# Kernel tuning notes

Measured on AMD Instinct MI355X. Metric: run time of the kernel, lower is better.

The kernel has to match this reference:

```python
import jax, jax.numpy as jnp
import numpy as np

H = 16  # hidden_size
IN = 1  # input_size

def setup_inputs() -> dict:
    key = jax.random.key(0)
    ks = jax.random.split(key, 7)
    B, T = 2048, 2048
    s_ih = 1.0 / np.sqrt(H)
    return {
        "x": jax.random.normal(ks[0], (B, T, IN), dtype=jnp.float32),
        # PyTorch LSTM param layout: [4H, in] / [4H, H], gate order i,f,g,o
        "W_ih": jax.random.uniform(ks[1], (4 * H, IN), jnp.float32, -s_ih, s_ih),
        "W_hh": jax.random.uniform(ks[2], (4 * H, H), jnp.float32, -s_ih, s_ih),
        "b_ih": jax.random.uniform(ks[3], (4 * H,), jnp.float32, -s_ih, s_ih),
        "b_hh": jax.random.uniform(ks[4], (4 * H,), jnp.float32, -s_ih, s_ih),
        "W_fc": jax.random.uniform(ks[5], (1, H), jnp.float32, -s_ih, s_ih),
        "b_fc": jax.random.uniform(ks[6], (1,), jnp.float32, -s_ih, s_ih),
    }

def reference(x, W_ih, W_hh, b_ih, b_hh, W_fc, b_fc):
    B = x.shape[0]
    # Precompute input contribution for all timesteps: [T, B, 4H]
    xg = jnp.swapaxes(x, 0, 1) @ W_ih.T + (b_ih + b_hh)

    def step(carry, xt):
        h, c = carry
        g = xt + h @ W_hh.T  # [B, 4H]
        i, f, gg, o = jnp.split(g, 4, axis=-1)  # PyTorch gate order i,f,g,o
        i = jax.nn.sigmoid(i)
        f = jax.nn.sigmoid(f)
        gg = jnp.tanh(gg)
        o = jax.nn.sigmoid(o)
        c = f * c + i * gg
        h = o * jnp.tanh(c)
        return (h, c), None

    h0 = jnp.zeros((B, H), x.dtype)
    (h_last, _), _ = jax.lax.scan(step, (h0, h0), xg)
    # fc applied only to last timestep's hidden state (x[:, -1, :] in torch)
    return h_last @ W_fc.T + b_fc
```

## Files before the change

### kernel.cpp

```cpp
#include <hip/hip_runtime.h>


__device__ __forceinline__ float i2f(int i) { return __int_as_float(i); }
__device__ __forceinline__ int   f2i(float f) { return __float_as_int(f); }

#define LOG2E 1.44269504088896340736f

#define FMAC_DPP(acc, h_, w_, n)                                               \
    asm("v_fmac_f32_dpp %0, %1, %2 row_ror:" #n " row_mask:0xf bank_mask:0xf"  \
        : "+v"(acc) : "v"(h_), "v"(w_));
#define MUL_DPP(dst, h_, w_, n)                                                \
    asm("v_mul_f32_dpp %0, %1, %2 row_ror:" #n " row_mask:0xf bank_mask:0xf"   \
        : "=v"(dst) : "v"(h_), "v"(w_));

#define STEP(s_imm) {                                                        \
    float xs_ = i2f(__builtin_amdgcn_readlane(f2i(xblk), (s_imm)));          \
    float aA_ = fmaf(wih_s, xs_, bias_s);                                    \
    aA_ = fmaf(hcur, w[0], aA_);                                             \
    FMAC_DPP(aA_, hcur, w[1], 1)                                             \
    FMAC_DPP(aA_, hcur, w[2], 2)                                             \
    FMAC_DPP(aA_, hcur, w[3], 3)                                             \
    FMAC_DPP(aA_, hcur, w[4], 4)                                             \
    FMAC_DPP(aA_, hcur, w[5], 5)                                             \
    FMAC_DPP(aA_, hcur, w[6], 6)                                             \
    FMAC_DPP(aA_, hcur, w[7], 7)                                             \
    float aB_;                                                               \
    MUL_DPP(aB_, hcur, w[8], 8)                                              \
    FMAC_DPP(aB_, hcur, w[9],  9)                                            \
    FMAC_DPP(aB_, hcur, w[10], 10)                                           \
    FMAC_DPP(aB_, hcur, w[11], 11)                                           \
    FMAC_DPP(aB_, hcur, w[12], 12)                                           \
    FMAC_DPP(aB_, hcur, w[13], 13)                                           \
    FMAC_DPP(aB_, hcur, w[14], 14)                                           \
    FMAC_DPP(aB_, hcur, w[15], 15)                                           \
    float acc_ = aA_ + aB_;                                                  \
    float e_   = __builtin_amdgcn_exp2f(acc_);               \
    float r_   = __builtin_amdgcn_rcpf(1.0f + e_);                           \
    float act_ = fmaf(aco, r_, bco);                                         \
    int   ai_  = f2i(act_);                                                  \
    float gi_  = i2f(__builtin_amdgcn_ds_bpermute(addr_i, ai_));             \
    float gf_  = i2f(__builtin_amdgcn_ds_bpermute(addr_f, ai_));             \
    float gg_  = i2f(__builtin_amdgcn_ds_bpermute(addr_g, ai_));             \
    float go_  = i2f(__builtin_amdgcn_ds_bpermute(addr_o, ai_));             \
    c = fmaf(gf_, c, gi_ * gg_);                \
    float e2_ = __builtin_amdgcn_exp2f(c);                                   \
    float r2_ = __builtin_amdgcn_rcpf(1.0f + e2_);                           \
    float th_ = fmaf(2.0f, r2_, -1.0f);                                      \
    hcur = go_ * th_;                                                        \
}

#define STEP8(base) STEP(base+0) STEP(base+1) STEP(base+2) STEP(base+3) \
                    STEP(base+4) STEP(base+5) STEP(base+6) STEP(base+7)

__global__ __launch_bounds__(256, 2)
__attribute__((amdgpu_waves_per_eu(2, 2)))
void lstm_fused(
    const float* __restrict__ x,
    const float* __restrict__ Wih,
    const float* __restrict__ Whh,
    const float* __restrict__ bih,
    const float* __restrict__ bhh,
    const float* __restrict__ Wfc,
    const float* __restrict__ bfc,
    float* __restrict__ out)
{
    const int T   = 2048;
    const int tid = blockIdx.x * blockDim.x + threadIdx.x;
    const int b   = tid >> 6;
    const int l   = threadIdx.x & 63;
    const int j   = l & 15;
    const int gate = l >> 4;

    int probe = __builtin_amdgcn_mov_dpp(j, 0x121, 0xF, 0xF, true);
    const int dir = (probe == ((j + 1) & 15)) ? 1 : -1;

    const float mco = (gate == 2) ? (-2.0f * LOG2E) : (-LOG2E);
    const float aco = (gate == 2) ? (-4.0f * LOG2E) : 1.0f;
    const float bco = (gate == 2) ? ( 2.0f * LOG2E) : 0.0f;

    float w[16];
#pragma unroll
    for (int s = 0; s < 16; ++s) {
        int k = (j + s * dir + 32) & 15;
        w[s] = Whh[l * 16 + k] * mco;
    }

    const float wih_s  = Wih[l] * mco;
    const float bias_s = (bih[l] + bhh[l]) * mco;

    const int addr_i = (j     ) << 2;
    const int addr_f = (j + 16) << 2;
    const int addr_g = (j + 32) << 2;
    const int addr_o = (j + 48) << 2;

    const float* xp = x + (size_t)b * T;
    float xblk = xp[l];

    float hcur = 0.0f, c = 0.0f;

#pragma unroll 1
    for (int blk = 0; blk < 32; ++blk) {
        const int nxt = (blk < 31) ? (blk + 1) : 31;
        float xnext = xp[nxt * 64 + l];
        STEP8(0) STEP8(8) STEP8(16) STEP8(24)
        STEP8(32) STEP8(40) STEP8(48) STEP8(56)
        xblk = xnext;
    }

    float p = hcur * (Wfc[j] * 0.25f);
    p += __shfl_xor(p, 32);
    p += __shfl_xor(p, 16);
    p += __shfl_xor(p, 8);
    p += __shfl_xor(p, 4);
    p += __shfl_xor(p, 2);
    p += __shfl_xor(p, 1);
    if (l == 0) out[b] = p + bfc[0];
}

extern "C" void kernel_launch(void* const* d_in, const int* in_sizes, int n_in,
                              void* d_out, int out_size, void* d_ws, size_t ws_size,
                              hipStream_t stream) {
    const float* x   = (const float*)d_in[0];
    const float* Wih = (const float*)d_in[1];
    const float* Whh = (const float*)d_in[2];
    const float* bih = (const float*)d_in[3];
    const float* bhh = (const float*)d_in[4];
    const float* Wfc = (const float*)d_in[5];
    const float* bfc = (const float*)d_in[6];
    float* out = (float*)d_out;

    const int B = 2048;
    const int threads = 256;
    const int blocks = (B * 64) / threads;
    hipLaunchKernelGGL(lstm_fused, dim3(blocks), dim3(threads), 0, stream,
                       x, Wih, Whh, bih, bhh, Wfc, bfc, out);
}
```

Measured before the change: 403.7 us.

## Interleave two batch sequences per wavefront to hide recurrence latency

```diff
diff --git a/kernel.cpp b/kernel.cpp
--- a/kernel.cpp
+++ b/kernel.cpp
@@ -13,47 +13,59 @@
     asm("v_mul_f32_dpp %0, %1, %2 row_ror:" #n " row_mask:0xf bank_mask:0xf"   \
         : "=v"(dst) : "v"(h_), "v"(w_));
 
-#define STEP(s_imm) {                                                        \
-    float xs_ = i2f(__builtin_amdgcn_readlane(f2i(xblk), (s_imm)));          \
-    float aA_ = fmaf(wih_s, xs_, bias_s);                                    \
-    aA_ = fmaf(hcur, w[0], aA_);                                             \
-    FMAC_DPP(aA_, hcur, w[1], 1)                                             \
-    FMAC_DPP(aA_, hcur, w[2], 2)                                             \
-    FMAC_DPP(aA_, hcur, w[3], 3)                                             \
-    FMAC_DPP(aA_, hcur, w[4], 4)                                             \
-    FMAC_DPP(aA_, hcur, w[5], 5)                                             \
-    FMAC_DPP(aA_, hcur, w[6], 6)                                             \
-    FMAC_DPP(aA_, hcur, w[7], 7)                                             \
-    float aB_;                                                               \
-    MUL_DPP(aB_, hcur, w[8], 8)                                              \
-    FMAC_DPP(aB_, hcur, w[9],  9)                                            \
-    FMAC_DPP(aB_, hcur, w[10], 10)                                           \
-    FMAC_DPP(aB_, hcur, w[11], 11)                                           \
-    FMAC_DPP(aB_, hcur, w[12], 12)                                           \
-    FMAC_DPP(aB_, hcur, w[13], 13)                                           \
-    FMAC_DPP(aB_, hcur, w[14], 14)                                           \
-    FMAC_DPP(aB_, hcur, w[15], 15)                                           \
-    float acc_ = aA_ + aB_;                                                  \
-    float e_   = __builtin_amdgcn_exp2f(acc_);               \
-    float r_   = __builtin_amdgcn_rcpf(1.0f + e_);                           \
-    float act_ = fmaf(aco, r_, bco);                                         \
-    int   ai_  = f2i(act_);                                                  \
-    float gi_  = i2f(__builtin_amdgcn_ds_bpermute(addr_i, ai_));             \
-    float gf_  = i2f(__builtin_amdgcn_ds_bpermute(addr_f, ai_));             \
-    float gg_  = i2f(__builtin_amdgcn_ds_bpermute(addr_g, ai_));             \
-    float go_  = i2f(__builtin_amdgcn_ds_bpermute(addr_o, ai_));             \
-    c = fmaf(gf_, c, gi_ * gg_);                \
-    float e2_ = __builtin_amdgcn_exp2f(c);                                   \
-    float r2_ = __builtin_amdgcn_rcpf(1.0f + e2_);                           \
-    float th_ = fmaf(2.0f, r2_, -1.0f);                                      \
-    hcur = go_ * th_;                                                        \
+#define STEP2(s_expr) {                                                      \
+    float xsA_ = i2f(__builtin_amdgcn_readlane(f2i(xblkA), (s_expr)));       \
+    float xsB_ = i2f(__builtin_amdgcn_readlane(f2i(xblkB), (s_expr)));       \
+    float aAl_ = fmaf(wih_s, xsA_, bias_s);                                  \
+    float aBl_ = fmaf(wih_s, xsB_, bias_s);                                  \
+    float aAh_, aBh_;                                                        \
+    aAl_ = fmaf(hA, w[0], aAl_);                                             \
+    aBl_ = fmaf(hB, w[0], aBl_);                                             \
+    MUL_DPP(aAh_, hA, w[8], 8)    MUL_DPP(aBh_, hB, w[8], 8)                 \
+    FMAC_DPP(aAl_, hA, w[1], 1)   FMAC_DPP(aBl_, hB, w[1], 1)                \
+    FMAC_DPP(aAh_, hA, w[9], 9)   FMAC_DPP(aBh_, hB, w[9], 9)                \
+    FMAC_DPP(aAl_, hA, w[2], 2)   FMAC_DPP(aBl_, hB, w[2], 2)                \
+    FMAC_DPP(aAh_, hA, w[10],10)  FMAC_DPP(aBh_, hB, w[10],10)               \
+    FMAC_DPP(aAl_, hA, w[3], 3)   FMAC_DPP(aBl_, hB, w[3], 3)                \
+    FMAC_DPP(aAh_, hA, w[11],11)  FMAC_DPP(aBh_, hB, w[11],11)               \
+    FMAC_DPP(aAl_, hA, w[4], 4)   FMAC_DPP(aBl_, hB, w[4], 4)                \
+    FMAC_DPP(aAh_, hA, w[12],12)  FMAC_DPP(aBh_, hB, w[12],12)               \
+    FMAC_DPP(aAl_, hA, w[5], 5)   FMAC_DPP(aBl_, hB, w[5], 5)                \
+    FMAC_DPP(aAh_, hA, w[13],13)  FMAC_DPP(aBh_, hB, w[13],13)               \
+    FMAC_DPP(aAl_, hA, w[6], 6)   FMAC_DPP(aBl_, hB, w[6], 6)                \
+    FMAC_DPP(aAh_, hA, w[14],14)  FMAC_DPP(aBh_, hB, w[14],14)               \
+    FMAC_DPP(aAl_, hA, w[7], 7)   FMAC_DPP(aBl_, hB, w[7], 7)                \
+    FMAC_DPP(aAh_, hA, w[15],15)  FMAC_DPP(aBh_, hB, w[15],15)               \
+    float accA_ = aAl_ + aAh_;                                               \
+    float accB_ = aBl_ + aBh_;                                               \
+    float eA_ = __builtin_amdgcn_exp2f(accA_);               \
+    float eB_ = __builtin_amdgcn_exp2f(accB_);                               \
+    float rA_ = __builtin_amdgcn_rcpf(1.0f + eA_);                           \
+    float rB_ = __builtin_amdgcn_rcpf(1.0f + eB_);                           \
+    float actA_ = fmaf(aco, rA_, bco);                                       \
+    float actB_ = fmaf(aco, rB_, bco);                                       \
+    int aiA_ = f2i(actA_); int aiB_ = f2i(actB_);                            \
+    float giA_ = i2f(__builtin_amdgcn_ds_bpermute(addr_i, aiA_));            \
+    float giB_ = i2f(__builtin_amdgcn_ds_bpermute(addr_i, aiB_));            \
+    float gfA_ = i2f(__builtin_amdgcn_ds_bpermute(addr_f, aiA_));            \
+    float gfB_ = i2f(__builtin_amdgcn_ds_bpermute(addr_f, aiB_));            \
+    float ggA_ = i2f(__builtin_amdgcn_ds_bpermute(addr_g, aiA_));            \
+    float ggB_ = i2f(__builtin_amdgcn_ds_bpermute(addr_g, aiB_));            \
+    float goA_ = i2f(__builtin_amdgcn_ds_bpermute(addr_o, aiA_));            \
+    float goB_ = i2f(__builtin_amdgcn_ds_bpermute(addr_o, aiB_));            \
+    cA = fmaf(gfA_, cA, giA_ * ggA_);               \
+    cB = fmaf(gfB_, cB, giB_ * ggB_);                                        \
+    float o2A_ = goA_ + goA_;                                 \
+    float o2B_ = goB_ + goB_;                                                \
+    float e2A_ = __builtin_amdgcn_exp2f(cA);                                 \
+    float e2B_ = __builtin_amdgcn_exp2f(cB);                                 \
+    float r2A_ = __builtin_amdgcn_rcpf(1.0f + e2A_);                         \
+    float r2B_ = __builtin_amdgcn_rcpf(1.0f + e2B_);                         \
+    hA = fmaf(o2A_, r2A_, -goA_);                \
+    hB = fmaf(o2B_, r2B_, -goB_);                                            \
 }
 
-#define STEP8(base) STEP(base+0) STEP(base+1) STEP(base+2) STEP(base+3) \
-                    STEP(base+4) STEP(base+5) STEP(base+6) STEP(base+7)
-
-__global__ __launch_bounds__(256, 2)
-__attribute__((amdgpu_waves_per_eu(2, 2)))
+__global__ __launch_bounds__(256)
 void lstm_fused(
     const float* __restrict__ x,
     const float* __restrict__ Wih,
@@ -65,8 +77,9 @@
     float* __restrict__ out)
 {
     const int T   = 2048;
-    const int tid = blockIdx.x * blockDim.x + threadIdx.x;
-    const int b   = tid >> 6;
+    const int wid = (blockIdx.x * blockDim.x + threadIdx.x) >> 6;
+    const int b0  = wid * 2;
+    const int b1  = b0 + 1;
     const int l   = threadIdx.x & 63;
     const int j   = l & 15;
     const int gate = l >> 4;
@@ -93,28 +106,45 @@
     const int addr_g = (j + 32) << 2;
     const int addr_o = (j + 48) << 2;
 
-    const float* xp = x + (size_t)b * T;
-    float xblk = xp[l];
+    const float* xpA = x + (size_t)b0 * T;
+    const float* xpB = x + (size_t)b1 * T;
+    float xblkA = xpA[l];
+    float xblkB = xpB[l];
 
-    float hcur = 0.0f, c = 0.0f;
+    float hA = 0.0f, cA = 0.0f;
+    float hB = 0.0f, cB = 0.0f;
 
 #pragma unroll 1
     for (int blk = 0; blk < 32; ++blk) {
         const int nxt = (blk < 31) ? (blk + 1) : 31;
-        float xnext = xp[nxt * 64 + l];
-        STEP8(0) STEP8(8) STEP8(16) STEP8(24)
-        STEP8(32) STEP8(40) STEP8(48) STEP8(56)
-        xblk = xnext;
+        float xnA = xpA[nxt * 64 + l];
+        float xnB = xpB[nxt * 64 + l];
+#pragma unroll 1
+        for (int sub = 0; sub < 4; ++sub) {
+            const int base = sub << 4;
+#pragma unroll
+            for (int k = 0; k < 16; ++k) {
+                STEP2(base + k)
+            }
+        }
+        xblkA = xnA;
+        xblkB = xnB;
     }
 
-    float p = hcur * (Wfc[j] * 0.25f);
-    p += __shfl_xor(p, 32);
-    p += __shfl_xor(p, 16);
-    p += __shfl_xor(p, 8);
-    p += __shfl_xor(p, 4);
-    p += __shfl_xor(p, 2);
-    p += __shfl_xor(p, 1);
-    if (l == 0) out[b] = p + bfc[0];
+    const float wf = Wfc[j] * 0.25f;
+    float pA = hA * wf;
+    float pB = hB * wf;
+    pA += __shfl_xor(pA, 32);  pB += __shfl_xor(pB, 32);
+    pA += __shfl_xor(pA, 16);  pB += __shfl_xor(pB, 16);
+    pA += __shfl_xor(pA, 8);   pB += __shfl_xor(pB, 8);
+    pA += __shfl_xor(pA, 4);   pB += __shfl_xor(pB, 4);
+    pA += __shfl_xor(pA, 2);   pB += __shfl_xor(pB, 2);
+    pA += __shfl_xor(pA, 1);   pB += __shfl_xor(pB, 1);
+    if (l == 0) {
+        float bb = bfc[0];
+        out[b0] = pA + bb;
+        out[b1] = pB + bb;
+    }
 }
 
 extern "C" void kernel_launch(void* const* d_in, const int* in_sizes, int n_in,
@@ -131,7 +161,7 @@
 
     const int B = 2048;
     const int threads = 256;
-    const int blocks = (B * 64) / threads;
+    const int blocks  = (B / 2) * 64 / threads;
     hipLaunchKernelGGL(lstm_fused, dim3(blocks), dim3(threads), 0, stream,
                        x, Wih, Whh, bih, bhh, Wfc, bfc, out);
 }
```

Result: slower. 482.4 us (+19.5%).
